# Kernel optimization log

Measured on AMD Instinct MI355X. Metric: run time of the kernel, lower is better.

Reference implementation:

```python
import jax, jax.numpy as jnp
import numpy as np

D_MODEL = 1536
NUM_HEADS = 16
QUERY_GROUPS = 4
HEAD_DIM = D_MODEL // NUM_HEADS  # 96
HEADS_PER_GROUP = NUM_HEADS // QUERY_GROUPS
THETA = 10000.0


def _grid_positions(grid_t, grid_h, grid_w):
    # [N, 3] lookup table of (t, h, w) coords, N = T*H*W, 'ij' meshgrid order
    t, h, w = jnp.meshgrid(jnp.arange(grid_t), jnp.arange(grid_h), jnp.arange(grid_w), indexing='ij')
    return jnp.stack([t.reshape(-1), h.reshape(-1), w.reshape(-1)], axis=-1)


def _rope3d(x, positions):
    # x: [B, N, H, head_dim]; rotate three contiguous head_dim//3 slices, one per axis
    B, N, H, hd = x.shape
    dpa = hd // 3            # dims per axis
    P = dpa // 2             # rotation pairs per axis
    freqs = 1.0 / (THETA ** (jnp.arange(P, dtype=jnp.float32) * 2.0 / dpa))  # same for t/h/w
    parts = []
    for axis in range(3):
        ang = positions[:, axis].astype(jnp.float32)[:, None] * freqs[None, :]  # [N, P]
        cos = jnp.cos(ang)[None, :, None, :]  # [1, N, 1, P]
        sin = jnp.sin(ang)[None, :, None, :]
        sl = x[..., axis * dpa:(axis + 1) * dpa].reshape(B, N, H, P, 2)
        x0, x1 = sl[..., 0], sl[..., 1]
        rot = jnp.stack([x0 * cos - x1 * sin, x0 * sin + x1 * cos], axis=-1)
        parts.append(rot.reshape(B, N, H, dpa))
    return jnp.concatenate(parts, axis=-1)


def setup_inputs() -> dict:
    key = jax.random.key(0)
    k1, k2, k3 = jax.random.split(key, 3)
    B, GT, GH, GW = 2, 8, 16, 16
    N = GT * GH * GW  # 2048
    x = jax.random.normal(k1, (B, N, D_MODEL), dtype=jnp.float32)
    qkv_out = NUM_HEADS * HEAD_DIM + 2 * QUERY_GROUPS * HEAD_DIM  # 2304
    w_qkv = jax.random.normal(k2, (qkv_out, D_MODEL), dtype=jnp.float32) * 0.02
    w_o = jax.random.normal(k3, (D_MODEL, D_MODEL), dtype=jnp.float32) * 0.02
    return {"x": x, "w_qkv": w_qkv, "w_o": w_o, "grid_t": GT, "grid_h": GH, "grid_w": GW}


def reference(x, w_qkv, w_o, grid_t, grid_h, grid_w):
    B, N, _ = x.shape
    qkv = x @ w_qkv.T  # [B, N, 2304]
    q_dim = NUM_HEADS * HEAD_DIM
    kv_dim = QUERY_GROUPS * HEAD_DIM
    q = qkv[..., :q_dim].reshape(B, N, NUM_HEADS, HEAD_DIM)
    k = qkv[..., q_dim:q_dim + kv_dim].reshape(B, N, QUERY_GROUPS, HEAD_DIM)
    v = qkv[..., q_dim + kv_dim:].reshape(B, N, QUERY_GROUPS, HEAD_DIM)

    pos = _grid_positions(grid_t, grid_h, grid_w)  # [N, 3]
    q = _rope3d(q, pos)
    k = _rope3d(k, pos)

    # GQA: repeat_interleave kv heads up to num_heads
    k = jnp.repeat(k, HEADS_PER_GROUP, axis=2)
    v = jnp.repeat(v, HEADS_PER_GROUP, axis=2)

    scale = 1.0 / jnp.sqrt(jnp.asarray(HEAD_DIM, dtype=x.dtype))
    scores = jnp.einsum('bnhd,bmhd->bhnm', q, k) * scale
    attn = jax.nn.softmax(scores, axis=-1)
    out = jnp.einsum('bhnm,bmhd->bnhd', attn, v).reshape(B, N, D_MODEL)
    return out @ w_o.T
```

## Files before the change

### kernel.cpp

```cpp
#include <hip/hip_runtime.h>
#include <hip/hip_bf16.h>

typedef short bf16x8 __attribute__((ext_vector_type(8)));
typedef float f32x4  __attribute__((ext_vector_type(4)));

#define NH    16
#define NG    4
#define HD    96
#define DM    1536
#define BB    2
#define NSEQ  2048
#define QKVD  2304
#define MROWS (BB * NSEQ)

__device__ __forceinline__ short bf16_bits(float v)
{
    __hip_bfloat16 h = __float2bfloat16(v);
    return *reinterpret_cast<short*>(&h);
}

__device__ __forceinline__ void stage16(short* dst, const float* src)
{
    float f[16];
    *(float4*)(f + 0)  = *(const float4*)(src + 0);
    *(float4*)(f + 4)  = *(const float4*)(src + 4);
    *(float4*)(f + 8)  = *(const float4*)(src + 8);
    *(float4*)(f + 12) = *(const float4*)(src + 12);
    bf16x8 v0, v1;
    #pragma unroll
    for (int j = 0; j < 8; ++j) { v0[j] = bf16_bits(f[j]); v1[j] = bf16_bits(f[8 + j]); }
    *(bf16x8*)dst = v0;
    *(bf16x8*)(dst + 8) = v1;
}
__device__ __forceinline__ void stage16(short* dst, const __hip_bfloat16* src)
{
    *(bf16x8*)dst       = *(const bf16x8*)src;
    *(bf16x8*)(dst + 8) = *(const bf16x8*)(src + 8);
}

__device__ __forceinline__ void store_c(__hip_bfloat16* p, float v)
{
    *p = __float2bfloat16(v);
}
__device__ __forceinline__ void store_c(float* p, float v) { *p = v; }

__device__ __forceinline__ void gload_lds16(const short* g, short* lds)
{
    __builtin_amdgcn_global_load_lds(
        (const __attribute__((address_space(1))) unsigned int*)g,
        (__attribute__((address_space(3))) unsigned int*)lds,
        16, 0, 0);
}

__global__ __launch_bounds__(256) void cvt3_bf16(
    const float* __restrict__ x,  short* __restrict__ xb,
    const float* __restrict__ wq, short* __restrict__ wqb,
    const float* __restrict__ wo, short* __restrict__ wob)
{
    const int i = blockIdx.x * 256 + threadIdx.x;
    const float* s; short* d; int off;
    if (i < 786432)       { s = x;  d = xb;  off = i; }
    else if (i < 1228800) { s = wq; d = wqb; off = i - 786432; }
    else                  { s = wo; d = wob; off = i - 1228800; }
    float f[8];
    *(float4*)(f + 0) = *(const float4*)(s + (size_t)off * 8);
    *(float4*)(f + 4) = *(const float4*)(s + (size_t)off * 8 + 4);
    bf16x8 v;
    #pragma unroll
    for (int j = 0; j < 8; ++j) v[j] = bf16_bits(f[j]);
    *(bf16x8*)(d + (size_t)off * 8) = v;
}

template <typename TC>
__global__ __launch_bounds__(256) void gemm_async(
    const short* __restrict__ A,
    const short* __restrict__ B,
    TC* __restrict__ C,
    int M, int Nc, int K, int lda, int ldb, int nbx)
{
    __shared__ __align__(16) short As[128][32];
    __shared__ __align__(16) short Bs[128][32];

    const int tid  = threadIdx.x;
    const int wave = tid >> 6;
    const int lane = tid & 63;
    const int quad = lane >> 4;
    const int l16  = lane & 15;
    const int wm = (wave >> 1) * 64;
    const int wn = (wave & 1) * 64;

    const int cpx = gridDim.x >> 3;
    const int swz = (blockIdx.x & 7) * cpx + (blockIdx.x >> 3);
    const int bx  = swz % nbx;
    const int by  = swz / nbx;
    const int m0 = by * 128;
    const int n0 = bx * 128;

    const int lrow = lane >> 2;
    const int lcol = (lane & 3) * 8;

    f32x4 acc[4][4] = {};

    for (int k0 = 0; k0 < K; k0 += 32) {
        __syncthreads();
        #pragma unroll
        for (int i = 0; i < 2; ++i) {
            const int j = wave * 2 + i;
            gload_lds16(A + (size_t)(m0 + j * 16 + lrow) * lda + k0 + lcol, &As[j * 16][0]);
            gload_lds16(B + (size_t)(n0 + j * 16 + lrow) * ldb + k0 + lcol, &Bs[j * 16][0]);
        }
        __syncthreads();

        bf16x8 af[4], bfr[4];
        #pragma unroll
        for (int i = 0; i < 4; ++i)
            af[i] = *(const bf16x8*)&As[wm + i * 16 + l16][quad * 8];
        #pragma unroll
        for (int j = 0; j < 4; ++j)
            bfr[j] = *(const bf16x8*)&Bs[wn + j * 16 + l16][quad * 8];
        #pragma unroll
        for (int i = 0; i < 4; ++i)
            #pragma unroll
            for (int j = 0; j < 4; ++j)
                acc[i][j] = __builtin_amdgcn_mfma_f32_16x16x32_bf16(
                    af[i], bfr[j], acc[i][j], 0, 0, 0);
    }

    #pragma unroll
    for (int i = 0; i < 4; ++i)
      #pragma unroll
      for (int j = 0; j < 4; ++j)
        #pragma unroll
        for (int r = 0; r < 4; ++r) {
            const int row = m0 + wm + i * 16 + quad * 4 + r;
            const int col = n0 + wn + j * 16 + l16;
            store_c(C + (size_t)row * Nc + col, acc[i][j][r]);
        }
}

#define KSTR 40

template <typename TA, typename TB, typename TC>
__global__ __launch_bounds__(256) void gemm_tiled(
    const TA* __restrict__ A,
    const TB* __restrict__ B,
    TC* __restrict__ C,
    int M, int Nc, int K, int lda)
{
    __shared__ __align__(16) short As[128][KSTR];
    __shared__ __align__(16) short Bs[128][KSTR];

    const int tid  = threadIdx.x;
    const int wave = tid >> 6;
    const int lane = tid & 63;
    const int quad = lane >> 4;
    const int l16  = lane & 15;
    const int wm = (wave >> 1) * 64;
    const int wn = (wave & 1) * 64;
    const int m0 = blockIdx.y * 128;
    const int n0 = blockIdx.x * 128;

    const int srow  = tid >> 1;
    const int skseg = (tid & 1) << 4;
    const TA* Asrc = A + (size_t)(m0 + srow) * lda + skseg;
    const TB* Bsrc = B + (size_t)(n0 + srow) * K + skseg;

    f32x4 acc[4][4] = {};

    for (int k0 = 0; k0 < K; k0 += 32) {
        __syncthreads();
        stage16(&As[srow][skseg], Asrc + k0);
        stage16(&Bs[srow][skseg], Bsrc + k0);
        __syncthreads();

        bf16x8 af[4], bfr[4];
        #pragma unroll
        for (int i = 0; i < 4; ++i)
            af[i] = *(const bf16x8*)&As[wm + i * 16 + l16][quad * 8];
        #pragma unroll
        for (int j = 0; j < 4; ++j)
            bfr[j] = *(const bf16x8*)&Bs[wn + j * 16 + l16][quad * 8];
        #pragma unroll
        for (int i = 0; i < 4; ++i)
            #pragma unroll
            for (int j = 0; j < 4; ++j)
                acc[i][j] = __builtin_amdgcn_mfma_f32_16x16x32_bf16(
                    af[i], bfr[j], acc[i][j], 0, 0, 0);
    }

    #pragma unroll
    for (int i = 0; i < 4; ++i)
      #pragma unroll
      for (int j = 0; j < 4; ++j)
        #pragma unroll
        for (int r = 0; r < 4; ++r) {
            const int row = m0 + wm + i * 16 + quad * 4 + r;
            const int col = n0 + wn + j * 16 + l16;
            store_c(C + (size_t)row * Nc + col, acc[i][j][r]);
        }
}

__global__ __launch_bounds__(256) void rope_inplace(__hip_bfloat16* qkv)
{
    const int e = blockIdx.x * 256 + threadIdx.x;
    if (e >= MROWS * 20 * 48) return;
    const int p2   = e % 48;
    const int t2   = e / 48;
    const int slot = t2 % 20;
    const int r    = t2 / 20;
    const int n    = r & (NSEQ - 1);

    const int pt = n >> 8;
    const int ph = (n >> 4) & 15;
    const int pw = n & 15;

    const int axis = p2 >> 4;
    const int lp   = p2 & 15;
    const int d0   = axis * 32 + 2 * lp;
    const int pos  = (axis == 0) ? pt : ((axis == 1) ? ph : pw);

    const int col = (slot < 16) ? (slot * HD + d0)
                                : (DM + (slot - 16) * HD + d0);
    __hip_bfloat16* p = qkv + (size_t)r * QKVD + col;

    const float x0 = __bfloat162float(p[0]);
    const float x1 = __bfloat162float(p[1]);
    const float freq = exp2f(-(float)lp * 0.8304820237f);
    float s, c;
    sincosf((float)pos * freq, &s, &c);
    p[0] = __float2bfloat16(x0 * c - x1 * s);
    p[1] = __float2bfloat16(x0 * s + x1 * c);
}

#define KVSTRIDE 196608

__global__ __launch_bounds__(256) void kv_scatter(
    const __hip_bfloat16* __restrict__ qkv,
    short* __restrict__ Kbuf,
    short* __restrict__ Vtbuf)
{
    const int tid = threadIdx.x;
    const int n0  = blockIdx.x * 64;
    const int bg  = blockIdx.y;
    const int b = bg >> 2, g = bg & 3;
    const size_t qbase = (size_t)(b * NSEQ + n0) * QKVD;

    for (int s = tid; s < 768; s += 256) {
        const int row = s / 12;
        const int c   = (s - row * 12) * 8;
        bf16x8 v = *(const bf16x8*)(qkv + qbase + (size_t)row * QKVD + DM + g * HD + c);
        *(bf16x8*)(Kbuf + (size_t)bg * KVSTRIDE + (size_t)(n0 + row) * HD + c) = v;
    }

    const int row  = tid & 63;
    const int dseg = (tid >> 6) * 24;
    const __hip_bfloat16* vsrc =
        qkv + qbase + (size_t)row * QKVD + DM + NG * HD + g * HD + dseg;
    short* vdst = Vtbuf + (size_t)bg * KVSTRIDE + n0 + row;
    #pragma unroll
    for (int u8 = 0; u8 < 3; ++u8) {
        short tmp[8];
        *(bf16x8*)tmp = *(const bf16x8*)(vsrc + u8 * 8);
        #pragma unroll
        for (int u = 0; u < 8; ++u)
            vdst[(size_t)(dseg + u8 * 8 + u) * NSEQ] = tmp[u];
    }
}

#define QT 64
#define KC 64
#define KSTR2 104
#define VSTR 72
#define PSTR 72

__global__ __launch_bounds__(256) void flash_attn(
    __hip_bfloat16* __restrict__ qkv,
    const short* __restrict__ Kbuf,
    const short* __restrict__ Vtbuf)
{
    __shared__ __align__(16) short Ks[KC][KSTR2];
    __shared__ __align__(16) short Vt[HD][VSTR];
    __shared__ __align__(16) short Pw[4][16][PSTR];

    const int tid  = threadIdx.x;
    const int wave = tid >> 6;
    const int lane = tid & 63;
    const int quad = lane >> 4;
    const int l16  = lane & 15;
    const int bh = blockIdx.y;
    const int b = bh >> 4, h = bh & 15;
    const int g = h >> 2;
    const int bg = b * NG + g;
    const int n0 = blockIdx.x * QT;

    const __hip_bfloat16* Qb = qkv + (size_t)(b * NSEQ + n0 + wave * 16) * QKVD + h * HD;
    const short* Kc = Kbuf  + (size_t)bg * KVSTRIDE;
    const short* Vc = Vtbuf + (size_t)bg * KVSTRIDE;

    bf16x8 qa[3];
    #pragma unroll
    for (int kk = 0; kk < 3; ++kk)
        qa[kk] = *(const bf16x8*)(Qb + (size_t)l16 * QKVD + kk * 32 + quad * 8);

    f32x4 o[6] = {};
    float psum[4] = {0.f, 0.f, 0.f, 0.f};
    const float c1 = 0.14724434f;
    const float c2 = -5.7707802f;
    const int sw = l16 >> 2;

    for (int j0 = 0; j0 < NSEQ; j0 += KC) {
        __syncthreads();
        for (int s = tid; s < 768; s += 256) {
            const int row = s / 12;
            const int c   = (s - row * 12) * 8;
            *(bf16x8*)&Ks[row][c] = *(const bf16x8*)(Kc + (size_t)j0 * HD + s * 8);
        }
        for (int s = tid; s < 768; s += 256) {
            const int d = s >> 3;
            const int c = (s & 7) * 8;
            *(bf16x8*)&Vt[d][c] = *(const bf16x8*)(Vc + (size_t)d * NSEQ + j0 + c);
        }
        __syncthreads();

        f32x4 S[4] = {};
        #pragma unroll
        for (int nt = 0; nt < 4; ++nt)
            #pragma unroll
            for (int kk = 0; kk < 3; ++kk) {
                bf16x8 kf = *(const bf16x8*)&Ks[nt * 16 + l16][kk * 32 + quad * 8];
                S[nt] = __builtin_amdgcn_mfma_f32_16x16x32_bf16(qa[kk], kf, S[nt], 0, 0, 0);
            }

        #pragma unroll
        for (int nt = 0; nt < 4; ++nt) {
            const int cb   = nt * 2 + (l16 >> 3);
            const int colp = ((cb ^ quad) << 3) + (l16 & 7);
            #pragma unroll
            for (int r = 0; r < 4; ++r) {
                const float p = exp2f(fmaf(S[nt][r], c1, c2));
                psum[r] += p;
                Pw[wave][quad * 4 + r][colp] = bf16_bits(p);
            }
        }

        bf16x8 pa0 = *(const bf16x8*)&Pw[wave][l16][(quad ^ sw) << 3];
        bf16x8 pa1 = *(const bf16x8*)&Pw[wave][l16][((quad ^ sw) + 4) << 3];
        #pragma unroll
        for (int dt = 0; dt < 6; ++dt) {
            bf16x8 vb0 = *(const bf16x8*)&Vt[dt * 16 + l16][quad * 8];
            bf16x8 vb1 = *(const bf16x8*)&Vt[dt * 16 + l16][32 + quad * 8];
            o[dt] = __builtin_amdgcn_mfma_f32_16x16x32_bf16(pa0, vb0, o[dt], 0, 0, 0);
            o[dt] = __builtin_amdgcn_mfma_f32_16x16x32_bf16(pa1, vb1, o[dt], 0, 0, 0);
        }
    }

    #pragma unroll
    for (int off = 1; off < 16; off <<= 1)
        #pragma unroll
        for (int r = 0; r < 4; ++r)
            psum[r] += __shfl_xor(psum[r], off);
    float inv_l[4];
    #pragma unroll
    for (int r = 0; r < 4; ++r) inv_l[r] = 1.f / psum[r];

    #pragma unroll
    for (int dt = 0; dt < 6; ++dt)
        #pragma unroll
        for (int r = 0; r < 4; ++r) {
            __hip_bfloat16* op =
                qkv + (size_t)(b * NSEQ + n0 + wave * 16 + quad * 4 + r) * QKVD
                    + h * HD + dt * 16 + l16;
            *op = __float2bfloat16(o[dt][r] * inv_l[r]);
        }
}

extern "C" void kernel_launch(void* const* d_in, const int* in_sizes, int n_in,
                              void* d_out, int out_size, void* d_ws, size_t ws_size,
                              hipStream_t stream)
{
    const float* x    = (const float*)d_in[0];
    const float* wqkv = (const float*)d_in[1];
    const float* wo   = (const float*)d_in[2];

    __hip_bfloat16* qkv = (__hip_bfloat16*)d_ws;
    short* xb    = (short*)d_out;
    short* wqb   = (short*)((char*)d_out + 12582912);
    short* Kbuf  = (short*)d_out;
    short* Vtbuf = (short*)((char*)d_out + 3145728);

    const bool wo_in_ws = ws_size >= 23592960;
    short* wob = wo_in_ws ? (short*)((char*)d_ws + 18874368) : (short*)d_out;

    cvt3_bf16<<<wo_in_ws ? 5952 : 4800, 256, 0, stream>>>(x, xb, wqkv, wqb, wo, wob);

    gemm_async<__hip_bfloat16>
        <<<(QKVD / 128) * (MROWS / 128), 256, 0, stream>>>(
            xb, wqb, qkv, MROWS, QKVD, DM, DM, DM, QKVD / 128);

    rope_inplace<<<(MROWS * 20 * 48) / 256, 256, 0, stream>>>(qkv);
    kv_scatter<<<dim3(NSEQ / 64, BB * NG), 256, 0, stream>>>(qkv, Kbuf, Vtbuf);
    flash_attn<<<dim3(NSEQ / QT, BB * NH), 256, 0, stream>>>(qkv, Kbuf, Vtbuf);

    if (wo_in_ws) {
        gemm_async<float>
            <<<(DM / 128) * (MROWS / 128), 256, 0, stream>>>(
                (const short*)qkv, wob, (float*)d_out, MROWS, DM, DM, QKVD, DM, DM / 128);
    } else {
        gemm_tiled<__hip_bfloat16, float, float>
            <<<dim3(DM / 128, MROWS / 128), 256, 0, stream>>>(
                qkv, wo, (float*)d_out, MROWS, DM, DM, QKVD);
    }
}
```

Before: 306.5 us.

## Pre-swizzle K/V into MFMA fragment layout and stream via direct global-to-LDS loads

kv_scatter now writes K and transposed V in a tiled layout that matches the MFMA operand fragments, 512-element tiles indexed by lane*8. flash_attn copies each tile straight into LDS with gload_lds16 (split across waves for K and V), and reads the fragments as contiguous per-lane vectors instead of padded 2D arrays. The grid is flattened, with the group index in the low bits so the four heads sharing a KV group are scheduled next to each other and reuse K/V in cache. The goal is less address math, fewer bank conflicts and better L2 reuse. The cost is a more complex scatter with scattered 2-byte V stores.

```diff
diff --git a/kernel.cpp b/kernel.cpp
--- a/kernel.cpp
+++ b/kernel.cpp
@@ -246,31 +246,44 @@
     const size_t qbase = (size_t)(b * NSEQ + n0) * QKVD;
 
     for (int s = tid; s < 768; s += 256) {
-        const int row = s / 12;
-        const int c   = (s - row * 12) * 8;
-        bf16x8 v = *(const bf16x8*)(qkv + qbase + (size_t)row * QKVD + DM + g * HD + c);
-        *(bf16x8*)(Kbuf + (size_t)bg * KVSTRIDE + (size_t)(n0 + row) * HD + c) = v;
+        const int row  = s / 12;
+        const int c8   = s - row * 12;
+        const int kk   = c8 >> 2;
+        const int quad = c8 & 3;
+        const int n    = n0 + row;
+        bf16x8 v = *(const bf16x8*)(qkv + qbase + (size_t)row * QKVD + DM + g * HD + c8 * 8);
+        short* dst = Kbuf + (size_t)bg * KVSTRIDE
+                   + ((size_t)((n >> 4) * 3 + kk) << 9)
+                   + ((quad << 4) + (n & 15)) * 8;
+        *(bf16x8*)dst = v;
     }
 
     const int row  = tid & 63;
+    const int n    = n0 + row;
     const int dseg = (tid >> 6) * 24;
+    const int jj   = n & 63;
+    const int half = jj >> 5;
+    const int quad = (jj >> 3) & 3;
+    const int e    = jj & 7;
     const __hip_bfloat16* vsrc =
         qkv + qbase + (size_t)row * QKVD + DM + NG * HD + g * HD + dseg;
-    short* vdst = Vtbuf + (size_t)bg * KVSTRIDE + n0 + row;
+    short* vbase = Vtbuf + (size_t)bg * KVSTRIDE + ((size_t)((n >> 6) * 12) << 9);
     #pragma unroll
     for (int u8 = 0; u8 < 3; ++u8) {
         short tmp[8];
         *(bf16x8*)tmp = *(const bf16x8*)(vsrc + u8 * 8);
         #pragma unroll
-        for (int u = 0; u < 8; ++u)
-            vdst[(size_t)(dseg + u8 * 8 + u) * NSEQ] = tmp[u];
+        for (int u = 0; u < 8; ++u) {
+            const int d   = dseg + u8 * 8 + u;
+            const int dt  = d >> 4;
+            const int l16 = d & 15;
+            vbase[(((dt << 1) + half) << 9) + ((quad << 4) + l16) * 8 + e] = tmp[u];
+        }
     }
 }
 
 #define QT 64
 #define KC 64
-#define KSTR2 104
-#define VSTR 72
 #define PSTR 72
 
 __global__ __launch_bounds__(256) void flash_attn(
@@ -278,8 +291,8 @@
     const short* __restrict__ Kbuf,
     const short* __restrict__ Vtbuf)
 {
-    __shared__ __align__(16) short Ks[KC][KSTR2];
-    __shared__ __align__(16) short Vt[HD][VSTR];
+    __shared__ __align__(16) short KsLin[6144];
+    __shared__ __align__(16) short VtLin[6144];
     __shared__ __align__(16) short Pw[4][16][PSTR];
 
     const int tid  = threadIdx.x;
@@ -287,16 +300,19 @@
     const int lane = tid & 63;
     const int quad = lane >> 4;
     const int l16  = lane & 15;
-    const int bh = blockIdx.y;
-    const int b = bh >> 4, h = bh & 15;
-    const int g = h >> 2;
-    const int bg = b * NG + g;
-    const int n0 = blockIdx.x * QT;
-
-    const __hip_bfloat16* Qb = qkv + (size_t)(b * NSEQ + n0 + wave * 16) * QKVD + h * HD;
+
+    const int id  = blockIdx.x;
+    const int bg  = id & 7;
+    const int k   = id >> 3;
+    const int b   = bg >> 2, g = bg & 3;
+    const int h   = g * 4 + (k & 3);
+    const int n0  = (k >> 2) * QT;
+
     const short* Kc = Kbuf  + (size_t)bg * KVSTRIDE;
     const short* Vc = Vtbuf + (size_t)bg * KVSTRIDE;
-
+    const int lane8 = lane * 8;
+
+    const __hip_bfloat16* Qb = qkv + (size_t)(b * NSEQ + n0 + wave * 16) * QKVD + h * HD;
     bf16x8 qa[3];
     #pragma unroll
     for (int kk = 0; kk < 3; ++kk)
@@ -310,26 +326,30 @@
 
     for (int j0 = 0; j0 < NSEQ; j0 += KC) {
         __syncthreads();
-        for (int s = tid; s < 768; s += 256) {
-            const int row = s / 12;
-            const int c   = (s - row * 12) * 8;
-            *(bf16x8*)&Ks[row][c] = *(const bf16x8*)(Kc + (size_t)j0 * HD + s * 8);
-        }
-        for (int s = tid; s < 768; s += 256) {
-            const int d = s >> 3;
-            const int c = (s & 7) * 8;
-            *(bf16x8*)&Vt[d][c] = *(const bf16x8*)(Vc + (size_t)d * NSEQ + j0 + c);
+        {
+            const short* Kch = Kc + ((size_t)((j0 >> 4) * 3) << 9);
+            const short* Vch = Vc + ((size_t)((j0 >> 6) * 12) << 9);
+            const short* sb = (wave < 2) ? Kch : Vch;
+            short* db       = (wave < 2) ? KsLin : VtLin;
+            #pragma unroll
+            for (int i = 0; i < 6; ++i) {
+                const int t = (wave & 1) * 6 + i;
+                gload_lds16(sb + ((size_t)t << 9) + lane8, db + (t << 9));
+            }
         }
         __syncthreads();
 
         f32x4 S[4] = {};
         #pragma unroll
-        for (int nt = 0; nt < 4; ++nt)
-            #pragma unroll
-            for (int kk = 0; kk < 3; ++kk) {
-                bf16x8 kf = *(const bf16x8*)&Ks[nt * 16 + l16][kk * 32 + quad * 8];
-                S[nt] = __builtin_amdgcn_mfma_f32_16x16x32_bf16(qa[kk], kf, S[nt], 0, 0, 0);
-            }
+        for (int nt = 0; nt < 4; ++nt) {
+            bf16x8 kf[3];
+            #pragma unroll
+            for (int kk = 0; kk < 3; ++kk)
+                kf[kk] = *(const bf16x8*)&KsLin[((nt * 3 + kk) << 9) + lane8];
+            #pragma unroll
+            for (int kk = 0; kk < 3; ++kk)
+                S[nt] = __builtin_amdgcn_mfma_f32_16x16x32_bf16(qa[kk], kf[kk], S[nt], 0, 0, 0);
+        }
 
         #pragma unroll
         for (int nt = 0; nt < 4; ++nt) {
@@ -347,8 +367,8 @@
         bf16x8 pa1 = *(const bf16x8*)&Pw[wave][l16][((quad ^ sw) + 4) << 3];
         #pragma unroll
         for (int dt = 0; dt < 6; ++dt) {
-            bf16x8 vb0 = *(const bf16x8*)&Vt[dt * 16 + l16][quad * 8];
-            bf16x8 vb1 = *(const bf16x8*)&Vt[dt * 16 + l16][32 + quad * 8];
+            bf16x8 vb0 = *(const bf16x8*)&VtLin[((dt * 2 + 0) << 9) + lane8];
+            bf16x8 vb1 = *(const bf16x8*)&VtLin[((dt * 2 + 1) << 9) + lane8];
             o[dt] = __builtin_amdgcn_mfma_f32_16x16x32_bf16(pa0, vb0, o[dt], 0, 0, 0);
             o[dt] = __builtin_amdgcn_mfma_f32_16x16x32_bf16(pa1, vb1, o[dt], 0, 0, 0);
         }
@@ -399,7 +419,7 @@
 
     rope_inplace<<<(MROWS * 20 * 48) / 256, 256, 0, stream>>>(qkv);
     kv_scatter<<<dim3(NSEQ / 64, BB * NG), 256, 0, stream>>>(qkv, Kbuf, Vtbuf);
-    flash_attn<<<dim3(NSEQ / QT, BB * NH), 256, 0, stream>>>(qkv, Kbuf, Vtbuf);
+    flash_attn<<<dim3(NSEQ / QT * BB * NH, 1), 256, 0, stream>>>(qkv, Kbuf, Vtbuf);
 
     if (wo_in_ws) {
         gemm_async<float>
```

Result: faster. 284.1 us (-7.3%).
